# Optimization experiments

Measured on AMD Instinct MI355X. Metric: run time of the kernel, lower is better.

## Reference

```python
import jax, jax.numpy as jnp
import numpy as np

B, T, E, H = 2, 2048, 1024, 16
Dh = E // H  # head_size = 64


def setup_inputs() -> dict:
    key = jax.random.key(0)
    ks = jax.random.split(key, 6)
    s = E ** -0.5
    x = jax.random.normal(ks[0], (B, T, E), dtype=jnp.float32)
    Wq = jax.random.normal(ks[1], (H, E, Dh), dtype=jnp.float32) * s
    Wk = jax.random.normal(ks[2], (H, E, Dh), dtype=jnp.float32) * s
    Wv = jax.random.normal(ks[3], (H, E, Dh), dtype=jnp.float32) * s
    wo_w = jax.random.normal(ks[4], (E, E), dtype=jnp.float32) * s  # torch Linear weight [out,in]
    wo_b = jax.random.normal(ks[5], (E,), dtype=jnp.float32) * 0.01
    return {"x": x, "Wq": Wq, "Wk": Wk, "Wv": Wv, "wo_w": wo_w, "wo_b": wo_b}


def reference(x, Wq, Wk, Wv, wo_w, wo_b):
    # Batched equivalent of the per-head Python loop: project all heads at once.
    q = jnp.einsum('bte,hed->bhtd', x, Wq)
    k = jnp.einsum('bte,hed->bhtd', x, Wk)
    v = jnp.einsum('bte,hed->bhtd', x, Wv)
    scale = Dh ** -0.5
    scores = jnp.einsum('bhtd,bhsd->bhts', q, k) * scale  # [B,H,T,T]
    causal = jnp.tril(jnp.ones((T, T), dtype=bool))
    scores = jnp.where(causal, scores, jnp.finfo(scores.dtype).min)
    att = jax.nn.softmax(scores, axis=-1)
    out = jnp.einsum('bhts,bhsd->bhtd', att, v)  # [B,H,T,Dh]
    # concat heads (head order along last dim, matching torch.cat over heads)
    out = out.transpose(0, 2, 1, 3).reshape(B, T, E)
    return out @ wo_w.T + wo_b
```

## Files before the change

### kernel.cpp

```cpp
#include <hip/hip_runtime.h>

#define B_ 2
#define T_ 2048
#define E_ 1024
#define H_ 16
#define DH 64

typedef unsigned short u16;
typedef unsigned int u32;
typedef __bf16 bf16x8 __attribute__((ext_vector_type(8)));
typedef float f32x4 __attribute__((ext_vector_type(4)));

__device__ __forceinline__ u16 f2bf(float f) {
  u32 u = __builtin_bit_cast(u32, f);
  u = u + 0x7FFFu + ((u >> 16) & 1u);
  return (u16)(u >> 16);
}
__device__ __forceinline__ bf16x8 ldfrag(const u16* p) { return *(const bf16x8*)p; }

__device__ __forceinline__ void gload_lds16(const u16* g, u16* l) {
  __builtin_amdgcn_global_load_lds((const __attribute__((address_space(1))) u32*)g,
                                   (__attribute__((address_space(3))) u32*)l, 16, 0, 0);
}

__global__ __launch_bounds__(256) void k_conv_all(const float* __restrict__ x,
                                                  const float* __restrict__ Wq,
                                                  const float* __restrict__ Wk,
                                                  const float* __restrict__ Wv,
                                                  const float* __restrict__ wo_w,
                                                  u16* __restrict__ xb, u16* __restrict__ wT,
                                                  u16* __restrict__ woB) {
  __shared__ __align__(16) u16 Ls[64][68];
  const int t = threadIdx.x;
  const int bx = blockIdx.x;
  if (bx < 2048 || bx >= 2816) {
    const float* src = (bx < 2048) ? x : wo_w;
    u16* dst = (bx < 2048) ? xb : woB;
    u32 i = (((bx < 2048) ? bx : (bx - 2816)) * 256u + t) * 8u;
    float4 a = *(const float4*)(src + i);
    float4 b = *(const float4*)(src + i + 4);
    uint4 v;
    v.x = (u32)f2bf(a.x) | ((u32)f2bf(a.y) << 16);
    v.y = (u32)f2bf(a.z) | ((u32)f2bf(a.w) << 16);
    v.z = (u32)f2bf(b.x) | ((u32)f2bf(b.y) << 16);
    v.w = (u32)f2bf(b.z) | ((u32)f2bf(b.w) << 16);
    *(uint4*)(dst + i) = v;
    return;
  }
  const int idx = bx - 2048;
  const int e0 = (idx & 15) * 64;
  const int h = (idx >> 4) & 15;
  const int which = idx >> 8;
  const float* src = (which == 0) ? Wq : ((which == 1) ? Wk : Wv);
  const float scale = (which == 0) ? 0.18033688011112042f : 1.0f;
#pragma unroll
  for (int p = 0; p < 4; p++) {
    int id2 = p * 256 + t;
    int row = id2 >> 4, ch = id2 & 15;
    float4 v = *(const float4*)(src + ((size_t)h * E_ + e0 + row) * DH + ch * 4);
    uint2 pk;
    pk.x = (u32)f2bf(v.x * scale) | ((u32)f2bf(v.y * scale) << 16);
    pk.y = (u32)f2bf(v.z * scale) | ((u32)f2bf(v.w * scale) << 16);
    *(uint2*)(&Ls[row][ch * 4]) = pk;
  }
  __syncthreads();
  u16* dst = wT + ((size_t)which * H_ + h) * (DH * E_);
#pragma unroll
  for (int p = 0; p < 4; p++) {
    int id2 = p * 256 + t;
    int d = id2 >> 4, ec = id2 & 15;
    uint2 pk;
    pk.x = (u32)Ls[ec * 4 + 0][d] | ((u32)Ls[ec * 4 + 1][d] << 16);
    pk.y = (u32)Ls[ec * 4 + 2][d] | ((u32)Ls[ec * 4 + 3][d] << 16);
    *(uint2*)(dst + (size_t)d * E_ + e0 + ec * 4) = pk;
  }
}

__global__ __launch_bounds__(256, 3) void k_qkv(const u16* __restrict__ xb, const u16* __restrict__ wT,
                                                u16* __restrict__ Qb, u16* __restrict__ Kb,
                                                u16* __restrict__ VbT) {
  __shared__ __align__(16) u16 As[128 * 64];
  __shared__ __align__(16) u16 Bs[128 * 64];
  const int tid = threadIdx.x;
  const int w = tid >> 6, lane = tid & 63, quad = lane >> 4, lr = lane & 15;
  const int wr = w >> 1, wc = w & 1;
  const int t0 = blockIdx.x * 128;
  const int n0 = blockIdx.y * 128;
  const int sr = lane >> 3, sc = lane & 7;

  f32x4 acc[4][4];
  const f32x4 z4 = {0.f, 0.f, 0.f, 0.f};
#pragma unroll
  for (int i = 0; i < 4; i++)
#pragma unroll
    for (int j = 0; j < 4; j++) acc[i][j] = z4;

  for (int k0 = 0; k0 < E_; k0 += 64) {
    __syncthreads();
#pragma unroll
    for (int ii = 0; ii < 4; ii++) {
      int ra = w * 32 + ii * 8 + sr;
      gload_lds16(xb + (size_t)(t0 + ra) * E_ + k0 + ((sc ^ (ra & 7)) << 3),
                  As + (w * 32 + ii * 8) * 64);
      gload_lds16(wT + (size_t)(n0 + ra) * E_ + k0 + ((sc ^ (ra & 7)) << 3),
                  Bs + (w * 32 + ii * 8) * 64);
    }
    __syncthreads();
#pragma unroll
    for (int kk = 0; kk < 2; kk++) {
      bf16x8 af[4], bfv[4];
#pragma unroll
      for (int rt = 0; rt < 4; rt++) {
        int row = wr * 64 + rt * 16 + lr;
        af[rt] = ldfrag(As + row * 64 + (((kk * 4 + quad) ^ (row & 7)) << 3));
      }
#pragma unroll
      for (int ct = 0; ct < 4; ct++) {
        int row = wc * 64 + ct * 16 + lr;
        bfv[ct] = ldfrag(Bs + row * 64 + (((kk * 4 + quad) ^ (row & 7)) << 3));
      }
#pragma unroll
      for (int rt = 0; rt < 4; rt++)
#pragma unroll
        for (int ct = 0; ct < 4; ct++)
          acc[rt][ct] = __builtin_amdgcn_mfma_f32_16x16x32_bf16(af[rt], bfv[ct], acc[rt][ct], 0, 0, 0);
    }
  }

  const int qkv = n0 >> 10;
  if (qkv < 2) {
    u16* outp = (qkv == 0) ? Qb : Kb;
#pragma unroll
    for (int rt = 0; rt < 4; rt++)
#pragma unroll
      for (int ct = 0; ct < 4; ct++) {
        int n = n0 + wc * 64 + ct * 16 + lr;
        int h = (n >> 6) & 15, d = n & 63;
#pragma unroll
        for (int r = 0; r < 4; r++) {
          int t = t0 + wr * 64 + rt * 16 + quad * 4 + r;
          int bb = t >> 11, tt = t & 2047;
          outp[(((size_t)bb * H_ + h) * T_ + tt) * DH + d] = f2bf(acc[rt][ct][r]);
        }
      }
  } else {
#pragma unroll
    for (int rt = 0; rt < 4; rt++)
#pragma unroll
      for (int ct = 0; ct < 4; ct++) {
        int n = n0 + wc * 64 + ct * 16 + lr;
        int h = (n >> 6) & 15, d = n & 63;
        int t = t0 + wr * 64 + rt * 16 + quad * 4;
        int bb = t >> 11, tt = t & 2047;
        uint2 pk;
        pk.x = (u32)f2bf(acc[rt][ct][0]) | ((u32)f2bf(acc[rt][ct][1]) << 16);
        pk.y = (u32)f2bf(acc[rt][ct][2]) | ((u32)f2bf(acc[rt][ct][3]) << 16);
        *(uint2*)(VbT + (((size_t)bb * H_ + h) * DH + d) * T_ + tt) = pk;
      }
  }
}

__global__ __launch_bounds__(256, 4) void k_attn(const u16* __restrict__ Qb, const u16* __restrict__ Kb,
                                                 const u16* __restrict__ VbT, u16* __restrict__ AO) {
  __shared__ __align__(16) u16 Ks[4096];
  __shared__ __align__(16) u16 Vts[4096];
  __shared__ __align__(16) u16 Ps[4096];
  const int tid = threadIdx.x;
  const int w = tid >> 6, lane = tid & 63, quad = lane >> 4, lr = lane & 15;
  const int l7 = lr & 7;
  const int srow = lane >> 3, schunk = lane & 7;
  const int i = blockIdx.x;
  const int h = blockIdx.y, bb = blockIdx.z;
  const u16* qb = Qb + ((size_t)bb * H_ + h) * (size_t)(T_ * DH);
  const u16* kb = Kb + ((size_t)bb * H_ + h) * (size_t)(T_ * DH);
  const u16* vbT = VbT + ((size_t)bb * H_ + h) * (size_t)(T_ * DH);
  const f32x4 z4 = {0.f, 0.f, 0.f, 0.f};
  const float MFIX = 20.0f;

  for (int jb = 0; jb < 2; jb++) {
    const int qt = jb ? i : (31 - i);
    const int t0 = qt * 64;

    const u16* qrow = qb + (size_t)(t0 + w * 16 + lr) * DH;
    bf16x8 bq0 = ldfrag(qrow + quad * 8);
    bf16x8 bq1 = ldfrag(qrow + 32 + quad * 8);

    f32x4 o_acc[4];
#pragma unroll
    for (int dt = 0; dt < 4; dt++) o_acc[dt] = z4;
    float l_i = 0.f;

    for (int jt = 0; jt <= qt; jt++) {
      const int j0 = jt * 64;
      __syncthreads();
#pragma unroll
      for (int ii = 0; ii < 2; ii++) {
        int r = w * 16 + ii * 8 + srow;
        gload_lds16(kb + (size_t)(j0 + r) * DH + ((schunk ^ (r & 7)) << 3),
                    Ks + (w * 16 + ii * 8) * 64);
        gload_lds16(vbT + (size_t)r * T_ + j0 + ((schunk ^ (r & 7)) << 3),
                    Vts + (w * 16 + ii * 8) * 64);
      }
      __syncthreads();

      f32x4 s_acc[4];
#pragma unroll
      for (int st = 0; st < 4; st++) s_acc[st] = z4;
#pragma unroll
      for (int st = 0; st < 4; st++) {
        bf16x8 ak0 = ldfrag(Ks + (st * 16 + lr) * 64 + ((quad ^ l7) << 3));
        bf16x8 ak1 = ldfrag(Ks + (st * 16 + lr) * 64 + (((4 + quad) ^ l7) << 3));
        s_acc[st] = __builtin_amdgcn_mfma_f32_16x16x32_bf16(ak0, bq0, s_acc[st], 0, 0, 0);
        s_acc[st] = __builtin_amdgcn_mfma_f32_16x16x32_bf16(ak1, bq1, s_acc[st], 0, 0, 0);
      }

      if (jt == qt) {
        int qloc = w * 16 + lr;
#pragma unroll
        for (int st = 0; st < 4; st++) {
          int sbase = st * 16 + quad * 4;
#pragma unroll
          for (int r = 0; r < 4; r++)
            if (sbase + r > qloc) s_acc[st][r] = -__builtin_inff();
        }
      }

      float rsum = 0.f;
#pragma unroll
      for (int st = 0; st < 4; st++) {
        float p0 = __builtin_amdgcn_exp2f(s_acc[st][0] - MFIX);
        float p1 = __builtin_amdgcn_exp2f(s_acc[st][1] - MFIX);
        float p2 = __builtin_amdgcn_exp2f(s_acc[st][2] - MFIX);
        float p3 = __builtin_amdgcn_exp2f(s_acc[st][3] - MFIX);
        rsum += (p0 + p1) + (p2 + p3);
        uint2 pk;
        pk.x = (__builtin_bit_cast(u32, p0) >> 16) | (__builtin_bit_cast(u32, p1) & 0xffff0000u);
        pk.y = (__builtin_bit_cast(u32, p2) >> 16) | (__builtin_bit_cast(u32, p3) & 0xffff0000u);
        *(uint2*)(Ps + (w * 16 + lr) * 64 + (((st * 2 + (quad >> 1)) ^ l7) << 3) + ((quad & 1) << 2)) = pk;
      }
      l_i += rsum;

#pragma unroll
      for (int kk = 0; kk < 2; kk++) {
        bf16x8 bp = ldfrag(Ps + (w * 16 + lr) * 64 + (((kk * 4 + quad) ^ l7) << 3));
#pragma unroll
        for (int dt = 0; dt < 4; dt++) {
          bf16x8 av = ldfrag(Vts + (dt * 16 + lr) * 64 + (((kk * 4 + quad) ^ l7) << 3));
          o_acc[dt] = __builtin_amdgcn_mfma_f32_16x16x32_bf16(av, bp, o_acc[dt], 0, 0, 0);
        }
      }
    }

    l_i += __shfl_xor(l_i, 16);
    l_i += __shfl_xor(l_i, 32);
    float inv = 1.0f / l_i;
    int t = t0 + w * 16 + lr;
    u16* orow = AO + ((size_t)bb * T_ + t) * E_ + h * DH;
#pragma unroll
    for (int dt = 0; dt < 4; dt++) {
      uint2 pk;
      pk.x = (u32)f2bf(o_acc[dt][0] * inv) | ((u32)f2bf(o_acc[dt][1] * inv) << 16);
      pk.y = (u32)f2bf(o_acc[dt][2] * inv) | ((u32)f2bf(o_acc[dt][3] * inv) << 16);
      *(uint2*)(orow + dt * 16 + quad * 4) = pk;
    }
  }
}

__global__ __launch_bounds__(256, 4) void k_oproj(const u16* __restrict__ AO, const u16* __restrict__ woB,
                                                  const float* __restrict__ bias, float* __restrict__ out) {
  __shared__ __align__(16) u16 As[64 * 64];
  __shared__ __align__(16) u16 Bs[64 * 64];
  const int tid = threadIdx.x;
  const int w = tid >> 6, lane = tid & 63, quad = lane >> 4, lr = lane & 15;
  const int r0 = blockIdx.x * 64, n0 = blockIdx.y * 64;
  const int sr = lane >> 3, sc = lane & 7;

  f32x4 acc[4];
  const f32x4 z4 = {0.f, 0.f, 0.f, 0.f};
#pragma unroll
  for (int i = 0; i < 4; i++) acc[i] = z4;

  for (int k0 = 0; k0 < E_; k0 += 64) {
    __syncthreads();
#pragma unroll
    for (int ii = 0; ii < 2; ii++) {
      int ra = w * 16 + ii * 8 + sr;
      gload_lds16(AO + (size_t)(r0 + ra) * E_ + k0 + ((sc ^ (ra & 7)) << 3),
                  As + (w * 16 + ii * 8) * 64);
      gload_lds16(woB + (size_t)(n0 + ra) * E_ + k0 + ((sc ^ (ra & 7)) << 3),
                  Bs + (w * 16 + ii * 8) * 64);
    }
    __syncthreads();
#pragma unroll
    for (int kk = 0; kk < 2; kk++) {
      bf16x8 af[4], bfv;
#pragma unroll
      for (int rt = 0; rt < 4; rt++) {
        int row = rt * 16 + lr;
        af[rt] = ldfrag(As + row * 64 + (((kk * 4 + quad) ^ (row & 7)) << 3));
      }
      {
        int row = w * 16 + lr;
        bfv = ldfrag(Bs + row * 64 + (((kk * 4 + quad) ^ (row & 7)) << 3));
      }
#pragma unroll
      for (int rt = 0; rt < 4; rt++)
        acc[rt] = __builtin_amdgcn_mfma_f32_16x16x32_bf16(af[rt], bfv, acc[rt], 0, 0, 0);
    }
  }

  {
    int col = n0 + w * 16 + lr;
    float bv = bias[col];
#pragma unroll
    for (int rt = 0; rt < 4; rt++)
#pragma unroll
      for (int r = 0; r < 4; r++) {
        int row = r0 + rt * 16 + quad * 4 + r;
        out[(size_t)row * E_ + col] = acc[rt][r] + bv;
      }
  }
}

extern "C" void kernel_launch(void* const* d_in, const int* in_sizes, int n_in,
                              void* d_out, int out_size, void* d_ws, size_t ws_size,
                              hipStream_t stream) {
  const float* x = (const float*)d_in[0];
  const float* Wq = (const float*)d_in[1];
  const float* Wk = (const float*)d_in[2];
  const float* Wv = (const float*)d_in[3];
  const float* wo_w = (const float*)d_in[4];
  const float* wo_b = (const float*)d_in[5];
  float* out = (float*)d_out;
  char* ws = (char*)d_ws;

  u16* xb  = (u16*)(ws + 0);
  u16* wT  = (u16*)(ws + 8388608);
  u16* woB = (u16*)(ws + 14680064);
  u16* Qb  = (u16*)(ws + 16777216);
  u16* Kb  = (u16*)(ws + 25165824);
  u16* VbT = (u16*)(ws + 33554432);
  u16* AO  = (u16*)(ws + 41943040);

  k_conv_all<<<3328, 256, 0, stream>>>(x, Wq, Wk, Wv, wo_w, xb, wT, woB);
  k_qkv<<<dim3(32, 24), 256, 0, stream>>>(xb, wT, Qb, Kb, VbT);
  k_attn<<<dim3(16, 16, 2), 256, 0, stream>>>(Qb, Kb, VbT, AO);
  k_oproj<<<dim3(64, 16), 256, 0, stream>>>(AO, woB, wo_b, out);
}
```

Baseline: 174.8 us.

## Double-buffer K/V tiles and give each attention wave two query sub-tiles

```diff
diff --git a/kernel.cpp b/kernel.cpp
--- a/kernel.cpp
+++ b/kernel.cpp
@@ -160,10 +160,10 @@
   }
 }
 
-__global__ __launch_bounds__(256, 4) void k_attn(const u16* __restrict__ Qb, const u16* __restrict__ Kb,
+__global__ __launch_bounds__(128, 1) void k_attn(const u16* __restrict__ Qb, const u16* __restrict__ Kb,
                                                  const u16* __restrict__ VbT, u16* __restrict__ AO) {
-  __shared__ __align__(16) u16 Ks[4096];
-  __shared__ __align__(16) u16 Vts[4096];
+  __shared__ __align__(16) u16 Ks[2][4096];
+  __shared__ __align__(16) u16 Vts[2][4096];
   __shared__ __align__(16) u16 Ps[4096];
   const int tid = threadIdx.x;
   const int w = tid >> 6, lane = tid & 63, quad = lane >> 4, lr = lane & 15;
@@ -181,87 +181,132 @@
     const int qt = jb ? i : (31 - i);
     const int t0 = qt * 64;
 
-    const u16* qrow = qb + (size_t)(t0 + w * 16 + lr) * DH;
-    bf16x8 bq0 = ldfrag(qrow + quad * 8);
-    bf16x8 bq1 = ldfrag(qrow + 32 + quad * 8);
-
-    f32x4 o_acc[4];
-#pragma unroll
-    for (int dt = 0; dt < 4; dt++) o_acc[dt] = z4;
-    float l_i = 0.f;
-
+    bf16x8 bq[2][2];
+#pragma unroll
+    for (int nt = 0; nt < 2; nt++) {
+      const u16* qrow = qb + (size_t)(t0 + w * 32 + nt * 16 + lr) * DH;
+      bq[nt][0] = ldfrag(qrow + quad * 8);
+      bq[nt][1] = ldfrag(qrow + 32 + quad * 8);
+    }
+
+    f32x4 o_acc[4][2];
+#pragma unroll
+    for (int dt = 0; dt < 4; dt++) {
+      o_acc[dt][0] = z4;
+      o_acc[dt][1] = z4;
+    }
+    float l_i[2] = {0.f, 0.f};
+
+#pragma unroll
+    for (int ii = 0; ii < 4; ii++) {
+      int r = ii * 16 + w * 8 + srow;
+      gload_lds16(kb + (size_t)r * DH + ((schunk ^ (r & 7)) << 3),
+                  &Ks[0][(ii * 16 + w * 8) * 64]);
+      gload_lds16(vbT + (size_t)r * T_ + ((schunk ^ (r & 7)) << 3),
+                  &Vts[0][(ii * 16 + w * 8) * 64]);
+    }
+    __syncthreads();
+
+    int cur = 0;
     for (int jt = 0; jt <= qt; jt++) {
       const int j0 = jt * 64;
+      if (jt < qt) {
+        const int jn = j0 + 64;
+#pragma unroll
+        for (int ii = 0; ii < 4; ii++) {
+          int r = ii * 16 + w * 8 + srow;
+          gload_lds16(kb + (size_t)(jn + r) * DH + ((schunk ^ (r & 7)) << 3),
+                      &Ks[cur ^ 1][(ii * 16 + w * 8) * 64]);
+          gload_lds16(vbT + (size_t)r * T_ + jn + ((schunk ^ (r & 7)) << 3),
+                      &Vts[cur ^ 1][(ii * 16 + w * 8) * 64]);
+        }
+      }
+
+      f32x4 s_acc[4][2];
+#pragma unroll
+      for (int st = 0; st < 4; st++) {
+        s_acc[st][0] = z4;
+        s_acc[st][1] = z4;
+      }
+      __builtin_amdgcn_s_setprio(1);
+#pragma unroll
+      for (int st = 0; st < 4; st++) {
+        bf16x8 ak0 = ldfrag(&Ks[cur][(st * 16 + lr) * 64 + ((quad ^ l7) << 3)]);
+        bf16x8 ak1 = ldfrag(&Ks[cur][(st * 16 + lr) * 64 + (((4 + quad) ^ l7) << 3)]);
+#pragma unroll
+        for (int nt = 0; nt < 2; nt++) {
+          s_acc[st][nt] = __builtin_amdgcn_mfma_f32_16x16x32_bf16(ak0, bq[nt][0], s_acc[st][nt], 0, 0, 0);
+          s_acc[st][nt] = __builtin_amdgcn_mfma_f32_16x16x32_bf16(ak1, bq[nt][1], s_acc[st][nt], 0, 0, 0);
+        }
+      }
+      __builtin_amdgcn_s_setprio(0);
+
+      if (jt == qt) {
+#pragma unroll
+        for (int nt = 0; nt < 2; nt++) {
+          int qloc = w * 32 + nt * 16 + lr;
+#pragma unroll
+          for (int st = 0; st < 4; st++) {
+            int sbase = st * 16 + quad * 4;
+#pragma unroll
+            for (int r = 0; r < 4; r++)
+              if (sbase + r > qloc) s_acc[st][nt][r] = -__builtin_inff();
+          }
+        }
+      }
+
+#pragma unroll
+      for (int nt = 0; nt < 2; nt++) {
+        float rsum = 0.f;
+#pragma unroll
+        for (int st = 0; st < 4; st++) {
+          float p0 = __builtin_amdgcn_exp2f(s_acc[st][nt][0] - MFIX);
+          float p1 = __builtin_amdgcn_exp2f(s_acc[st][nt][1] - MFIX);
+          float p2 = __builtin_amdgcn_exp2f(s_acc[st][nt][2] - MFIX);
+          float p3 = __builtin_amdgcn_exp2f(s_acc[st][nt][3] - MFIX);
+          rsum += (p0 + p1) + (p2 + p3);
+          uint2 pk;
+          pk.x = (__builtin_bit_cast(u32, p0) >> 16) | (__builtin_bit_cast(u32, p1) & 0xffff0000u);
+          pk.y = (__builtin_bit_cast(u32, p2) >> 16) | (__builtin_bit_cast(u32, p3) & 0xffff0000u);
+          *(uint2*)(Ps + (w * 32 + nt * 16 + lr) * 64 +
+                    (((st * 2 + (quad >> 1)) ^ l7) << 3) + ((quad & 1) << 2)) = pk;
+        }
+        l_i[nt] += rsum;
+      }
+
+      __builtin_amdgcn_s_setprio(1);
+#pragma unroll
+      for (int kk = 0; kk < 2; kk++) {
+        bf16x8 bp0 = ldfrag(Ps + (w * 32 + lr) * 64 + (((kk * 4 + quad) ^ l7) << 3));
+        bf16x8 bp1 = ldfrag(Ps + (w * 32 + 16 + lr) * 64 + (((kk * 4 + quad) ^ l7) << 3));
+#pragma unroll
+        for (int dt = 0; dt < 4; dt++) {
+          bf16x8 av = ldfrag(&Vts[cur][(dt * 16 + lr) * 64 + (((kk * 4 + quad) ^ l7) << 3)]);
+          o_acc[dt][0] = __builtin_amdgcn_mfma_f32_16x16x32_bf16(av, bp0, o_acc[dt][0], 0, 0, 0);
+          o_acc[dt][1] = __builtin_amdgcn_mfma_f32_16x16x32_bf16(av, bp1, o_acc[dt][1], 0, 0, 0);
+        }
+      }
+      __builtin_amdgcn_s_setprio(0);
+
       __syncthreads();
-#pragma unroll
-      for (int ii = 0; ii < 2; ii++) {
-        int r = w * 16 + ii * 8 + srow;
-        gload_lds16(kb + (size_t)(j0 + r) * DH + ((schunk ^ (r & 7)) << 3),
-                    Ks + (w * 16 + ii * 8) * 64);
-        gload_lds16(vbT + (size_t)r * T_ + j0 + ((schunk ^ (r & 7)) << 3),
-                    Vts + (w * 16 + ii * 8) * 64);
-      }
-      __syncthreads();
-
-      f32x4 s_acc[4];
-#pragma unroll
-      for (int st = 0; st < 4; st++) s_acc[st] = z4;
-#pragma unroll
-      for (int st = 0; st < 4; st++) {
-        bf16x8 ak0 = ldfrag(Ks + (st * 16 + lr) * 64 + ((quad ^ l7) << 3));
-        bf16x8 ak1 = ldfrag(Ks + (st * 16 + lr) * 64 + (((4 + quad) ^ l7) << 3));
-        s_acc[st] = __builtin_amdgcn_mfma_f32_16x16x32_bf16(ak0, bq0, s_acc[st], 0, 0, 0);
-        s_acc[st] = __builtin_amdgcn_mfma_f32_16x16x32_bf16(ak1, bq1, s_acc[st], 0, 0, 0);
-      }
-
-      if (jt == qt) {
-        int qloc = w * 16 + lr;
-#pragma unroll
-        for (int st = 0; st < 4; st++) {
-          int sbase = st * 16 + quad * 4;
-#pragma unroll
-          for (int r = 0; r < 4; r++)
-            if (sbase + r > qloc) s_acc[st][r] = -__builtin_inff();
-        }
-      }
-
-      float rsum = 0.f;
-#pragma unroll
-      for (int st = 0; st < 4; st++) {
-        float p0 = __builtin_amdgcn_exp2f(s_acc[st][0] - MFIX);
-        float p1 = __builtin_amdgcn_exp2f(s_acc[st][1] - MFIX);
-        float p2 = __builtin_amdgcn_exp2f(s_acc[st][2] - MFIX);
-        float p3 = __builtin_amdgcn_exp2f(s_acc[st][3] - MFIX);
-        rsum += (p0 + p1) + (p2 + p3);
+      cur ^= 1;
+    }
+
+#pragma unroll
+    for (int nt = 0; nt < 2; nt++) {
+      float l = l_i[nt];
+      l += __shfl_xor(l, 16);
+      l += __shfl_xor(l, 32);
+      float inv = 1.0f / l;
+      int t = t0 + w * 32 + nt * 16 + lr;
+      u16* orow = AO + ((size_t)bb * T_ + t) * E_ + h * DH;
+#pragma unroll
+      for (int dt = 0; dt < 4; dt++) {
         uint2 pk;
-        pk.x = (__builtin_bit_cast(u32, p0) >> 16) | (__builtin_bit_cast(u32, p1) & 0xffff0000u);
-        pk.y = (__builtin_bit_cast(u32, p2) >> 16) | (__builtin_bit_cast(u32, p3) & 0xffff0000u);
-        *(uint2*)(Ps + (w * 16 + lr) * 64 + (((st * 2 + (quad >> 1)) ^ l7) << 3) + ((quad & 1) << 2)) = pk;
-      }
-      l_i += rsum;
-
-#pragma unroll
-      for (int kk = 0; kk < 2; kk++) {
-        bf16x8 bp = ldfrag(Ps + (w * 16 + lr) * 64 + (((kk * 4 + quad) ^ l7) << 3));
-#pragma unroll
-        for (int dt = 0; dt < 4; dt++) {
-          bf16x8 av = ldfrag(Vts + (dt * 16 + lr) * 64 + (((kk * 4 + quad) ^ l7) << 3));
-          o_acc[dt] = __builtin_amdgcn_mfma_f32_16x16x32_bf16(av, bp, o_acc[dt], 0, 0, 0);
-        }
-      }
-    }
-
-    l_i += __shfl_xor(l_i, 16);
-    l_i += __shfl_xor(l_i, 32);
-    float inv = 1.0f / l_i;
-    int t = t0 + w * 16 + lr;
-    u16* orow = AO + ((size_t)bb * T_ + t) * E_ + h * DH;
-#pragma unroll
-    for (int dt = 0; dt < 4; dt++) {
-      uint2 pk;
-      pk.x = (u32)f2bf(o_acc[dt][0] * inv) | ((u32)f2bf(o_acc[dt][1] * inv) << 16);
-      pk.y = (u32)f2bf(o_acc[dt][2] * inv) | ((u32)f2bf(o_acc[dt][3] * inv) << 16);
-      *(uint2*)(orow + dt * 16 + quad * 4) = pk;
+        pk.x = (u32)f2bf(o_acc[dt][nt][0] * inv) | ((u32)f2bf(o_acc[dt][nt][1] * inv) << 16);
+        pk.y = (u32)f2bf(o_acc[dt][nt][2] * inv) | ((u32)f2bf(o_acc[dt][nt][3] * inv) << 16);
+        *(uint2*)(orow + dt * 16 + quad * 4) = pk;
+      }
     }
   }
 }
@@ -344,6 +389,6 @@
 
   k_conv_all<<<3328, 256, 0, stream>>>(x, Wq, Wk, Wv, wo_w, xb, wT, woB);
   k_qkv<<<dim3(32, 24), 256, 0, stream>>>(xb, wT, Qb, Kb, VbT);
-  k_attn<<<dim3(16, 16, 2), 256, 0, stream>>>(Qb, Kb, VbT, AO);
+  k_attn<<<dim3(16, 16, 2), 128, 0, stream>>>(Qb, Kb, VbT, AO);
   k_oproj<<<dim3(64, 16), 256, 0, stream>>>(AO, woB, wo_b, out);
 }
```

Result: slower. 185.8 us (+6.3%).

## Load K/V fragments directly from global into registers, prefetch next K tile

Applied to the files above, without the earlier changes.

```diff
diff --git a/kernel.cpp b/kernel.cpp
--- a/kernel.cpp
+++ b/kernel.cpp
@@ -160,15 +160,12 @@
   }
 }
 
-__global__ __launch_bounds__(256, 4) void k_attn(const u16* __restrict__ Qb, const u16* __restrict__ Kb,
+__global__ __launch_bounds__(256, 2) void k_attn(const u16* __restrict__ Qb, const u16* __restrict__ Kb,
                                                  const u16* __restrict__ VbT, u16* __restrict__ AO) {
-  __shared__ __align__(16) u16 Ks[4096];
-  __shared__ __align__(16) u16 Vts[4096];
   __shared__ __align__(16) u16 Ps[4096];
   const int tid = threadIdx.x;
   const int w = tid >> 6, lane = tid & 63, quad = lane >> 4, lr = lane & 15;
   const int l7 = lr & 7;
-  const int srow = lane >> 3, schunk = lane & 7;
   const int i = blockIdx.x;
   const int h = blockIdx.y, bb = blockIdx.z;
   const u16* qb = Qb + ((size_t)bb * H_ + h) * (size_t)(T_ * DH);
@@ -177,6 +174,9 @@
   const f32x4 z4 = {0.f, 0.f, 0.f, 0.f};
   const float MFIX = 20.0f;
 
+  const u16* krow = kb + (size_t)lr * DH + quad * 8;
+  const u16* vrow = vbT + (size_t)lr * T_ + quad * 8;
+
   for (int jb = 0; jb < 2; jb++) {
     const int qt = jb ? i : (31 - i);
     const int t0 = qt * 64;
@@ -190,29 +190,33 @@
     for (int dt = 0; dt < 4; dt++) o_acc[dt] = z4;
     float l_i = 0.f;
 
+    bf16x8 ak0[4], ak1[4];
+#pragma unroll
+    for (int st = 0; st < 4; st++) {
+      ak0[st] = ldfrag(krow + (size_t)(st * 16) * DH);
+      ak1[st] = ldfrag(krow + (size_t)(st * 16) * DH + 32);
+    }
+
     for (int jt = 0; jt <= qt; jt++) {
       const int j0 = jt * 64;
-      __syncthreads();
-#pragma unroll
-      for (int ii = 0; ii < 2; ii++) {
-        int r = w * 16 + ii * 8 + srow;
-        gload_lds16(kb + (size_t)(j0 + r) * DH + ((schunk ^ (r & 7)) << 3),
-                    Ks + (w * 16 + ii * 8) * 64);
-        gload_lds16(vbT + (size_t)r * T_ + j0 + ((schunk ^ (r & 7)) << 3),
-                    Vts + (w * 16 + ii * 8) * 64);
-      }
-      __syncthreads();
+
+      bf16x8 av[4][2];
+#pragma unroll
+      for (int dt = 0; dt < 4; dt++) {
+        av[dt][0] = ldfrag(vrow + (size_t)(dt * 16) * T_ + j0);
+        av[dt][1] = ldfrag(vrow + (size_t)(dt * 16) * T_ + j0 + 32);
+      }
 
       f32x4 s_acc[4];
 #pragma unroll
       for (int st = 0; st < 4; st++) s_acc[st] = z4;
+      __builtin_amdgcn_s_setprio(1);
 #pragma unroll
       for (int st = 0; st < 4; st++) {
-        bf16x8 ak0 = ldfrag(Ks + (st * 16 + lr) * 64 + ((quad ^ l7) << 3));
-        bf16x8 ak1 = ldfrag(Ks + (st * 16 + lr) * 64 + (((4 + quad) ^ l7) << 3));
-        s_acc[st] = __builtin_amdgcn_mfma_f32_16x16x32_bf16(ak0, bq0, s_acc[st], 0, 0, 0);
-        s_acc[st] = __builtin_amdgcn_mfma_f32_16x16x32_bf16(ak1, bq1, s_acc[st], 0, 0, 0);
-      }
+        s_acc[st] = __builtin_amdgcn_mfma_f32_16x16x32_bf16(ak0[st], bq0, s_acc[st], 0, 0, 0);
+        s_acc[st] = __builtin_amdgcn_mfma_f32_16x16x32_bf16(ak1[st], bq1, s_acc[st], 0, 0, 0);
+      }
+      __builtin_amdgcn_s_setprio(0);
 
       if (jt == qt) {
         int qloc = w * 16 + lr;
@@ -240,15 +244,24 @@
       }
       l_i += rsum;
 
+      if (jt < qt) {
+        const u16* kn = krow + (size_t)(j0 + 64) * DH;
+#pragma unroll
+        for (int st = 0; st < 4; st++) {
+          ak0[st] = ldfrag(kn + (size_t)(st * 16) * DH);
+          ak1[st] = ldfrag(kn + (size_t)(st * 16) * DH + 32);
+        }
+      }
+
+      __builtin_amdgcn_s_setprio(1);
 #pragma unroll
       for (int kk = 0; kk < 2; kk++) {
         bf16x8 bp = ldfrag(Ps + (w * 16 + lr) * 64 + (((kk * 4 + quad) ^ l7) << 3));
 #pragma unroll
-        for (int dt = 0; dt < 4; dt++) {
-          bf16x8 av = ldfrag(Vts + (dt * 16 + lr) * 64 + (((kk * 4 + quad) ^ l7) << 3));
-          o_acc[dt] = __builtin_amdgcn_mfma_f32_16x16x32_bf16(av, bp, o_acc[dt], 0, 0, 0);
-        }
-      }
+        for (int dt = 0; dt < 4; dt++)
+          o_acc[dt] = __builtin_amdgcn_mfma_f32_16x16x32_bf16(av[dt][kk], bp, o_acc[dt], 0, 0, 0);
+      }
+      __builtin_amdgcn_s_setprio(0);
     }
 
     l_i += __shfl_xor(l_i, 16);
```

After: 244.1 us. 1.4x slower.

## Remap GEMM blocks per XCD and enlarge output-projection tile to 128x64

Applied to the files above, without the earlier changes.

```diff
diff --git a/kernel.cpp b/kernel.cpp
--- a/kernel.cpp
+++ b/kernel.cpp
@@ -84,8 +84,10 @@
   const int tid = threadIdx.x;
   const int w = tid >> 6, lane = tid & 63, quad = lane >> 4, lr = lane & 15;
   const int wr = w >> 1, wc = w & 1;
-  const int t0 = blockIdx.x * 128;
-  const int n0 = blockIdx.y * 128;
+  const int bid = blockIdx.x;
+  const int xcd = bid & 7, bidx = bid >> 3;
+  const int t0 = (xcd * 4 + bidx / 24) * 128;
+  const int n0 = (bidx % 24) * 128;
   const int sr = lane >> 3, sc = lane & 7;
 
   f32x4 acc[4][4];
@@ -266,58 +268,73 @@
   }
 }
 
-__global__ __launch_bounds__(256, 4) void k_oproj(const u16* __restrict__ AO, const u16* __restrict__ woB,
+__global__ __launch_bounds__(256, 3) void k_oproj(const u16* __restrict__ AO, const u16* __restrict__ woB,
                                                   const float* __restrict__ bias, float* __restrict__ out) {
-  __shared__ __align__(16) u16 As[64 * 64];
+  __shared__ __align__(16) u16 As[128 * 64];
   __shared__ __align__(16) u16 Bs[64 * 64];
   const int tid = threadIdx.x;
   const int w = tid >> 6, lane = tid & 63, quad = lane >> 4, lr = lane & 15;
-  const int r0 = blockIdx.x * 64, n0 = blockIdx.y * 64;
+  const int wr = w >> 1, wc = w & 1;
+  const int bid = blockIdx.x;
+  const int xcd = bid & 7, bidx = bid >> 3;
+  const int r0 = (xcd * 4 + (bidx >> 4)) * 128;
+  const int n0 = (bidx & 15) * 64;
   const int sr = lane >> 3, sc = lane & 7;
 
-  f32x4 acc[4];
+  f32x4 acc[4][2];
   const f32x4 z4 = {0.f, 0.f, 0.f, 0.f};
 #pragma unroll
-  for (int i = 0; i < 4; i++) acc[i] = z4;
+  for (int i = 0; i < 4; i++) {
+    acc[i][0] = z4;
+    acc[i][1] = z4;
+  }
 
   for (int k0 = 0; k0 < E_; k0 += 64) {
     __syncthreads();
 #pragma unroll
+    for (int ii = 0; ii < 4; ii++) {
+      int ra = w * 32 + ii * 8 + sr;
+      gload_lds16(AO + (size_t)(r0 + ra) * E_ + k0 + ((sc ^ (ra & 7)) << 3),
+                  As + (w * 32 + ii * 8) * 64);
+    }
+#pragma unroll
     for (int ii = 0; ii < 2; ii++) {
-      int ra = w * 16 + ii * 8 + sr;
-      gload_lds16(AO + (size_t)(r0 + ra) * E_ + k0 + ((sc ^ (ra & 7)) << 3),
-                  As + (w * 16 + ii * 8) * 64);
-      gload_lds16(woB + (size_t)(n0 + ra) * E_ + k0 + ((sc ^ (ra & 7)) << 3),
+      int rb = w * 16 + ii * 8 + sr;
+      gload_lds16(woB + (size_t)(n0 + rb) * E_ + k0 + ((sc ^ (rb & 7)) << 3),
                   Bs + (w * 16 + ii * 8) * 64);
     }
     __syncthreads();
 #pragma unroll
     for (int kk = 0; kk < 2; kk++) {
-      bf16x8 af[4], bfv;
+      bf16x8 af[4], bfv[2];
 #pragma unroll
       for (int rt = 0; rt < 4; rt++) {
-        int row = rt * 16 + lr;
+        int row = wr * 64 + rt * 16 + lr;
         af[rt] = ldfrag(As + row * 64 + (((kk * 4 + quad) ^ (row & 7)) << 3));
       }
-      {
-        int row = w * 16 + lr;
-        bfv = ldfrag(Bs + row * 64 + (((kk * 4 + quad) ^ (row & 7)) << 3));
+#pragma unroll
+      for (int ct = 0; ct < 2; ct++) {
+        int row = wc * 32 + ct * 16 + lr;
+        bfv[ct] = ldfrag(Bs + row * 64 + (((kk * 4 + quad) ^ (row & 7)) << 3));
       }
 #pragma unroll
       for (int rt = 0; rt < 4; rt++)
-        acc[rt] = __builtin_amdgcn_mfma_f32_16x16x32_bf16(af[rt], bfv, acc[rt], 0, 0, 0);
-    }
-  }
-
-  {
-    int col = n0 + w * 16 + lr;
+#pragma unroll
+        for (int ct = 0; ct < 2; ct++)
+          acc[rt][ct] = __builtin_amdgcn_mfma_f32_16x16x32_bf16(af[rt], bfv[ct], acc[rt][ct], 0, 0, 0);
+    }
+  }
+
+#pragma unroll
+  for (int ct = 0; ct < 2; ct++) {
+    int col = n0 + wc * 32 + ct * 16 + lr;
     float bv = bias[col];
 #pragma unroll
     for (int rt = 0; rt < 4; rt++)
 #pragma unroll
       for (int r = 0; r < 4; r++) {
-        int row = r0 + rt * 16 + quad * 4 + r;
-        out[(size_t)row * E_ + col] = acc[rt][r] + bv;
+        int row = r0 + wr * 64 + rt * 16 + quad * 4 + r;
+        out[(size_t)row * E_ + col] = acc[rt][ct][r] + bv;
       }
   }
 }
@@ -343,7 +360,7 @@
   u16* AO  = (u16*)(ws + 41943040);
 
   k_conv_all<<<3328, 256, 0, stream>>>(x, Wq, Wk, Wv, wo_w, xb, wT, woB);
-  k_qkv<<<dim3(32, 24), 256, 0, stream>>>(xb, wT, Qb, Kb, VbT);
+  k_qkv<<<768, 256, 0, stream>>>(xb, wT, Qb, Kb, VbT);
   k_attn<<<dim3(16, 16, 2), 256, 0, stream>>>(Qb, Kb, VbT, AO);
-  k_oproj<<<dim3(64, 16), 256, 0, stream>>>(AO, woB, wo_b, out);
-}
+  k_oproj<<<512, 256, 0, stream>>>(AO, woB, wo_b, out);
+}
```

Measured after the change: 179.9 us. 1.03x slower.
